# Kernel optimization log

Hardware: AMD Instinct MI355X
Metric: run time of the kernel (lower is better)

The kernel has to match this reference:

```python
import jax, jax.numpy as jnp
import numpy as np

N_NODES = 50000
N_EDGES = 800000
NUM_FEATURES = 256
HIDDEN = 128
NUM_CLASSES = 64


def gcn_conv(x, edge_index, W, b):
    """PyG-style GCNConv: out = D^-1/2 (A+I) D^-1/2 (x W) + b.

    edge_index[0] = source (j), edge_index[1] = target (i);
    messages flow source -> target and are summed at the target.
    """
    n = x.shape[0]
    loop = jnp.arange(n, dtype=edge_index.dtype)
    src = jnp.concatenate([edge_index[0], loop])  # [E+N]
    dst = jnp.concatenate([edge_index[1], loop])  # [E+N]

    h = x @ W  # [N, out_dim] — transform before propagate, as in PyG GCNConv

    deg = jax.ops.segment_sum(jnp.ones_like(dst, dtype=h.dtype), dst, num_segments=n)
    dinv = jnp.where(deg > 0, jax.lax.rsqrt(deg), 0.0)
    norm = dinv[src] * dinv[dst]  # [E+N]

    out = jax.ops.segment_sum(norm[:, None] * h[src], dst, num_segments=n)
    return out + b


def setup_inputs() -> dict:
    key = jax.random.key(0)
    k1, k2, k3, k4 = jax.random.split(key, 4)
    x = jax.random.normal(k1, (N_NODES, NUM_FEATURES), dtype=jnp.float32)
    edge_index = jax.random.randint(k2, (2, N_EDGES), 0, N_NODES, dtype=jnp.int64)
    # Glorot-style init for the two GCN layer weights, zero bias (PyG default)
    W1 = jax.random.normal(k3, (NUM_FEATURES, HIDDEN), dtype=jnp.float32) * (1.0 / np.sqrt(NUM_FEATURES))
    b1 = jnp.zeros((HIDDEN,), dtype=jnp.float32)
    W2 = jax.random.normal(k4, (HIDDEN, NUM_CLASSES), dtype=jnp.float32) * (1.0 / np.sqrt(HIDDEN))
    b2 = jnp.zeros((NUM_CLASSES,), dtype=jnp.float32)
    return {"x": x, "edge_index": edge_index, "W1": W1, "b1": b1, "W2": W2, "b2": b2}


def reference(x, edge_index, W1, b1, W2, b2):
    h = gcn_conv(x, edge_index, W1, b1)
    h = jax.nn.relu(h)
    # dropout(p=0.5, training=True): fixed key stands in for torch RNG
    keep = jax.random.bernoulli(jax.random.key(42), 0.5, h.shape)
    h = jnp.where(keep, h * 2.0, 0.0)
    out = gcn_conv(h, edge_index, W2, b2)
    return out
```

## Files before the change

### kernel.cpp

```cpp
#include <hip/hip_runtime.h>


typedef __attribute__((ext_vector_type(8))) short bf16x8;
typedef __attribute__((ext_vector_type(4))) float f32x4;
typedef __attribute__((ext_vector_type(8))) unsigned short us8;

__device__ __forceinline__ unsigned tf_rotl(unsigned x, int d) {
    return (x << d) | (x >> (32 - d));
}

__device__ __forceinline__ bool dropout_keep(unsigned flat_idx) {
    const unsigned K0 = 0u, K1 = 42u;
    const unsigned K2 = K0 ^ K1 ^ 0x1BD11BDAu;
    unsigned x0 = 0u, x1 = flat_idx;
    x0 += K0; x1 += K1;
#define TF_R(r) { x0 += x1; x1 = tf_rotl(x1, (r)); x1 ^= x0; }
    TF_R(13) TF_R(15) TF_R(26) TF_R(6)
    x0 += K1; x1 += K2 + 1u;
    TF_R(17) TF_R(29) TF_R(16) TF_R(24)
    x0 += K2; x1 += K0 + 2u;
    TF_R(13) TF_R(15) TF_R(26) TF_R(6)
    x0 += K0; x1 += K1 + 3u;
    TF_R(17) TF_R(29) TF_R(16) TF_R(24)
    x0 += K1; x1 += K2 + 4u;
    TF_R(13) TF_R(15) TF_R(26) TF_R(6)
    x0 += K2; x1 += K0 + 5u;
#undef TF_R
    return (((x0 ^ x1) >> 31) & 1u) == 0u;
}

__device__ __forceinline__ unsigned short bf16_rn(float x) {
    unsigned u = __float_as_uint(x);
    unsigned r = u + 0x7FFFu + ((u >> 16) & 1u);
    return (unsigned short)(r >> 16);
}
__device__ __forceinline__ void split_bf16(float x, unsigned short& h, unsigned short& l) {
    h = bf16_rn(x);
    float fh = __uint_as_float(((unsigned)h) << 16);
    l = bf16_rn(x - fh);
}
__device__ __forceinline__ void split4(float4 v, ushort4& h, ushort4& l) {
    unsigned short h0, h1, h2, h3, l0, l1, l2, l3;
    split_bf16(v.x, h0, l0); split_bf16(v.y, h1, l1);
    split_bf16(v.z, h2, l2); split_bf16(v.w, h3, l3);
    h = make_ushort4(h0, h1, h2, h3);
    l = make_ushort4(l0, l1, l2, l3);
}

__device__ __forceinline__ int ei_stride(const int* __restrict__ ei) {
    bool i64 = true;
#pragma unroll
    for (int k = 1; k <= 15; k += 2) i64 = i64 && (ei[k] == 0);
    return i64 ? 2 : 1;
}

__global__ void count_slot(const int* __restrict__ ei, unsigned* __restrict__ deg,
                           unsigned* __restrict__ aux, int E) {
    int e = blockIdx.x * blockDim.x + threadIdx.x;
    if (e >= E) return;
    size_t st = ei_stride(ei);
    aux[e] = atomicAdd(&deg[ei[((size_t)E + e) * st]], 1u);
}

__global__ __launch_bounds__(256)
void scan_phase1(const unsigned* __restrict__ deg, unsigned* __restrict__ blockSums,
                 float* __restrict__ dinv, int N) {
    const int i = blockIdx.x * 256 + threadIdx.x;
    const int lane = threadIdx.x & 63, wave = threadIdx.x >> 6;
    unsigned v = 0;
    if (i < N) {
        unsigned d = deg[i];
        v = (d + 7u) & ~7u;
        dinv[i] = rsqrtf((float)(d + 1u));
    }
    unsigned s = v;
#pragma unroll
    for (int o = 32; o > 0; o >>= 1) s += __shfl_down(s, o, 64);
    __shared__ unsigned ws[4];
    if (lane == 0) ws[wave] = s;
    __syncthreads();
    if (threadIdx.x == 0)
        blockSums[blockIdx.x] = ws[0] + ws[1] + ws[2] + ws[3];
}

__global__ __launch_bounds__(1024)
void scan_phase2(unsigned* __restrict__ blockSums, int nb) {
    __shared__ unsigned s[1024];
    const int t = threadIdx.x;
    unsigned v = (t < nb) ? blockSums[t] : 0u;
    s[t] = v;
    __syncthreads();
    for (int off = 1; off < 1024; off <<= 1) {
        unsigned u = (t >= off) ? s[t - off] : 0u;
        __syncthreads();
        s[t] += u;
        __syncthreads();
    }
    if (t < nb) blockSums[t] = s[t] - v;
}

__global__ __launch_bounds__(256)
void scan_phase3(const unsigned* __restrict__ deg, const unsigned* __restrict__ blockSums,
                 unsigned* __restrict__ rowptr, int* __restrict__ csr, int N) {
    const int i = blockIdx.x * 256 + threadIdx.x;
    const int t = threadIdx.x;
    unsigned d = 0, v = 0;
    if (i < N) {
        d = deg[i];
        v = (d + 7u) & ~7u;
    }
    __shared__ unsigned s[256];
    s[t] = v;
    __syncthreads();
    for (int off = 1; off < 256; off <<= 1) {
        unsigned u = (t >= off) ? s[t - off] : 0u;
        __syncthreads();
        s[t] += u;
        __syncthreads();
    }
    const unsigned incl = s[t];
    const unsigned off0 = blockSums[blockIdx.x];
    if (i < N) {
        const unsigned rp = off0 + incl - v;
        rowptr[i] = rp;
        if (i == N - 1) rowptr[N] = off0 + incl;
        for (unsigned u = d; u < v; ++u) csr[rp + u] = N;
    }
}

__global__ void place_edges(const int* __restrict__ ei, const unsigned* __restrict__ rowptr,
                            const unsigned* __restrict__ aux, int* __restrict__ csr, int E) {
    int e = blockIdx.x * blockDim.x + threadIdx.x;
    if (e >= E) return;
    size_t st = ei_stride(ei);
    int s = ei[(size_t)e * st];
    int d = ei[((size_t)E + e) * st];
    csr[rowptr[d] + aux[e]] = s;
}

__global__ void split_both(const float* __restrict__ W1, const float* __restrict__ W2,
                           unsigned short* __restrict__ wT1_hi, unsigned short* __restrict__ wT1_lo,
                           unsigned short* __restrict__ wT2_hi, unsigned short* __restrict__ wT2_lo) {
    int idx = blockIdx.x * blockDim.x + threadIdx.x;
    unsigned short h, l;
    if (idx < 256 * 128) {
        int k = idx / 128, n = idx % 128;
        split_bf16(W1[idx], h, l);
        wT1_hi[(size_t)n * 256 + k] = h;
        wT1_lo[(size_t)n * 256 + k] = l;
    } else if (idx < 256 * 128 + 128 * 64) {
        int j = idx - 256 * 128;
        int k = j / 64, n = j % 64;
        split_bf16(W2[j], h, l);
        wT2_hi[(size_t)n * 128 + k] = h;
        wT2_lo[(size_t)n * 128 + k] = l;
    }
}

template <int K_, int NOUT_, bool SPLITA>
__global__ __launch_bounds__(256)
void gemm_mfma(const void* __restrict__ Xv, const unsigned short* __restrict__ wT_hi,
               const unsigned short* __restrict__ wT_lo, const float* __restrict__ scale,
               unsigned short* __restrict__ Yb, int nrows) {
    constexpr int BM = 64, BK = 32, NKT = K_ / BK;
    constexpr int CT = NOUT_ / 64;
    constexpr int LDW = BK + 8;
    constexpr int WPT = NOUT_ / 32;

    __shared__ __attribute__((aligned(16))) unsigned short xs_hi[BM][LDW];
    __shared__ __attribute__((aligned(16))) unsigned short xs_lo[SPLITA ? BM : 1][SPLITA ? LDW : 1];
    __shared__ __attribute__((aligned(16))) unsigned short ws_hi[NOUT_][LDW];
    __shared__ __attribute__((aligned(16))) unsigned short ws_lo[NOUT_][LDW];

    const int t = threadIdx.x;
    const int wave = t >> 6, lane = t & 63;
    const int m16 = lane & 15, kg = lane >> 4;
    const int row0 = blockIdx.x * BM;
    const int n0 = wave * (16 * CT);

    if (blockIdx.x == 0 && t < NOUT_ / 8) {
        us8 z = (us8)0;
        *(us8*)&Yb[(size_t)nrows * NOUT_ + t * 8] = z;
    }

    const float* Xf = (const float*)Xv;
    const unsigned short* Xb = (const unsigned short*)Xv;

    f32x4 acc[4][CT];
#pragma unroll
    for (int r = 0; r < 4; ++r)
#pragma unroll
        for (int c = 0; c < CT; ++c) acc[r][c] = {0.f, 0.f, 0.f, 0.f};

    float4 xpre[2];
    us8 xpre_b;
    ushort4 wpre_h[WPT], wpre_l[WPT];

    if constexpr (SPLITA) {
#pragma unroll
        for (int i = 0; i < 2; ++i) {
            int idx = t + i * 256;
            int r = idx >> 3, c4 = idx & 7;
            int gr = row0 + r;
            xpre[i] = (gr < nrows) ? *(const float4*)&Xf[(size_t)gr * K_ + c4 * 4]
                                   : make_float4(0.f, 0.f, 0.f, 0.f);
        }
    } else {
        int r = t >> 2, c8 = t & 3;
        int gr = row0 + r;
        xpre_b = (gr < nrows) ? *(const us8*)&Xb[(size_t)gr * K_ + c8 * 8] : (us8)0;
    }
#pragma unroll
    for (int i = 0; i < WPT; ++i) {
        int idx = t + i * 256;
        int n = idx >> 3, c4 = idx & 7;
        wpre_h[i] = *(const ushort4*)&wT_hi[(size_t)n * K_ + c4 * 4];
        wpre_l[i] = *(const ushort4*)&wT_lo[(size_t)n * K_ + c4 * 4];
    }

    for (int kb = 0; kb < NKT; ++kb) {
        if constexpr (SPLITA) {
#pragma unroll
            for (int i = 0; i < 2; ++i) {
                int idx = t + i * 256;
                int r = idx >> 3, c4 = idx & 7;
                ushort4 h, l;
                split4(xpre[i], h, l);
                *(ushort4*)&xs_hi[r][c4 * 4] = h;
                *(ushort4*)&xs_lo[r][c4 * 4] = l;
            }
        } else {
            int r = t >> 2, c8 = t & 3;
            *(us8*)&xs_hi[r][c8 * 8] = xpre_b;
        }
#pragma unroll
        for (int i = 0; i < WPT; ++i) {
            int idx = t + i * 256;
            int n = idx >> 3, c4 = idx & 7;
            *(ushort4*)&ws_hi[n][c4 * 4] = wpre_h[i];
            *(ushort4*)&ws_lo[n][c4 * 4] = wpre_l[i];
        }
        __syncthreads();

        if (kb + 1 < NKT) {
            const int koff = (kb + 1) * BK;
            if constexpr (SPLITA) {
#pragma unroll
                for (int i = 0; i < 2; ++i) {
                    int idx = t + i * 256;
                    int r = idx >> 3, c4 = idx & 7;
                    int gr = row0 + r;
                    xpre[i] = (gr < nrows) ? *(const float4*)&Xf[(size_t)gr * K_ + koff + c4 * 4]
                                           : make_float4(0.f, 0.f, 0.f, 0.f);
                }
            } else {
                int r = t >> 2, c8 = t & 3;
                int gr = row0 + r;
                xpre_b = (gr < nrows) ? *(const us8*)&Xb[(size_t)gr * K_ + koff + c8 * 8] : (us8)0;
            }
#pragma unroll
            for (int i = 0; i < WPT; ++i) {
                int idx = t + i * 256;
                int n = idx >> 3, c4 = idx & 7;
                wpre_h[i] = *(const ushort4*)&wT_hi[(size_t)n * K_ + koff + c4 * 4];
                wpre_l[i] = *(const ushort4*)&wT_lo[(size_t)n * K_ + koff + c4 * 4];
            }
        }

        bf16x8 bh[CT], bl[CT];
#pragma unroll
        for (int c = 0; c < CT; ++c) {
            bh[c] = *(const bf16x8*)&ws_hi[n0 + c * 16 + m16][kg * 8];
            bl[c] = *(const bf16x8*)&ws_lo[n0 + c * 16 + m16][kg * 8];
        }
#pragma unroll
        for (int r = 0; r < 4; ++r) {
            bf16x8 ah = *(const bf16x8*)&xs_hi[r * 16 + m16][kg * 8];
            if constexpr (SPLITA) {
                bf16x8 al = *(const bf16x8*)&xs_lo[r * 16 + m16][kg * 8];
#pragma unroll
                for (int c = 0; c < CT; ++c) {
                    acc[r][c] = __builtin_amdgcn_mfma_f32_16x16x32_bf16(ah, bh[c], acc[r][c], 0, 0, 0);
                    acc[r][c] = __builtin_amdgcn_mfma_f32_16x16x32_bf16(ah, bl[c], acc[r][c], 0, 0, 0);
                    acc[r][c] = __builtin_amdgcn_mfma_f32_16x16x32_bf16(al, bh[c], acc[r][c], 0, 0, 0);
                }
            } else {
#pragma unroll
                for (int c = 0; c < CT; ++c) {
                    acc[r][c] = __builtin_amdgcn_mfma_f32_16x16x32_bf16(ah, bh[c], acc[r][c], 0, 0, 0);
                    acc[r][c] = __builtin_amdgcn_mfma_f32_16x16x32_bf16(ah, bl[c], acc[r][c], 0, 0, 0);
                }
            }
        }
        __syncthreads();
    }

#pragma unroll
    for (int r = 0; r < 4; ++r) {
#pragma unroll
        for (int j = 0; j < 4; ++j) {
            int gr = row0 + r * 16 + kg * 4 + j;
            if (gr < nrows) {
                float s = scale[gr];
#pragma unroll
                for (int c = 0; c < CT; ++c)
                    Yb[(size_t)gr * NOUT_ + n0 + c * 16 + m16] = bf16_rn(acc[r][c][j] * s);
            }
        }
    }
}

__global__ __launch_bounds__(256)
void gather_drop(const unsigned* __restrict__ hs , const int* __restrict__ csr,
                 const unsigned* __restrict__ rowptr, const float* __restrict__ dinv,
                 const float* __restrict__ bias, unsigned* __restrict__ outb ,
                 int N) {
    const int node = blockIdx.x * 4 + (threadIdx.x >> 6);
    if (node >= N) return;
    const int lane = threadIdx.x & 63;
    const unsigned beg = rowptr[node];
    const unsigned end = rowptr[node + 1];
    const float dn = dinv[node];

    unsigned v = hs[(size_t)node * 64 + lane];
    float ax = __uint_as_float(v << 16);
    float ay = __uint_as_float(v & 0xffff0000u);
    for (unsigned k = beg; k < end; k += 8) {
        int j[8];
#pragma unroll
        for (int u = 0; u < 8; ++u) j[u] = csr[k + u];
        unsigned w[8];
#pragma unroll
        for (int u = 0; u < 8; ++u) w[u] = hs[(size_t)j[u] * 64 + lane];
#pragma unroll
        for (int u = 0; u < 8; ++u) {
            ax += __uint_as_float(w[u] << 16);
            ay += __uint_as_float(w[u] & 0xffff0000u);
        }
    }
    const int f0 = 2 * lane;
    float o0 = fmaxf(dn * ax + bias[f0], 0.0f);
    float o1 = fmaxf(dn * ay + bias[f0 + 1], 0.0f);
    unsigned base = (unsigned)node * 128u + (unsigned)f0;
    o0 = dropout_keep(base) ? 2.0f * o0 : 0.0f;
    o1 = dropout_keep(base + 1u) ? 2.0f * o1 : 0.0f;
    outb[(size_t)node * 64 + lane] =
        (unsigned)bf16_rn(o0) | ((unsigned)bf16_rn(o1) << 16);
}

__global__ __launch_bounds__(256)
void gather_out(const unsigned short* __restrict__ hs , const int* __restrict__ csr,
                const unsigned* __restrict__ rowptr, const float* __restrict__ dinv,
                const float* __restrict__ bias, float* __restrict__ outp, int N) {
    const int node = blockIdx.x * 4 + (threadIdx.x >> 6);
    if (node >= N) return;
    const int lane = threadIdx.x & 63;
    const unsigned beg = rowptr[node];
    const unsigned end = rowptr[node + 1];
    const float dn = dinv[node];

    float acc = __uint_as_float(((unsigned)hs[(size_t)node * 64 + lane]) << 16);
    for (unsigned k = beg; k < end; k += 8) {
        int j[8];
#pragma unroll
        for (int u = 0; u < 8; ++u) j[u] = csr[k + u];
        unsigned short w[8];
#pragma unroll
        for (int u = 0; u < 8; ++u) w[u] = hs[(size_t)j[u] * 64 + lane];
#pragma unroll
        for (int u = 0; u < 8; ++u) acc += __uint_as_float(((unsigned)w[u]) << 16);
    }
    outp[(size_t)node * 64 + lane] = dn * acc + bias[lane];
}

extern "C" void kernel_launch(void* const* d_in, const int* in_sizes, int n_in,
                              void* d_out, int out_size, void* d_ws, size_t ws_size,
                              hipStream_t stream) {
    const float* x  = (const float*)d_in[0];
    const int*   ei = (const int*)d_in[1];
    const float* W1 = (const float*)d_in[2];
    const float* b1 = (const float*)d_in[3];
    const float* W2 = (const float*)d_in[4];
    const float* b2 = (const float*)d_in[5];
    float* out = (float*)d_out;

    const int Fdim = 256, Hdim = 128, Cdim = 64;
    const int N = in_sizes[0] / Fdim;
    const int E = in_sizes[1] / 2;
    const int CSR_CAP = E + 7 * N;
    const int NB = (N + 255) / 256;

    unsigned short* wT1_hi = (unsigned short*)d_ws;
    unsigned short* wT1_lo = wT1_hi + 256 * 128;
    unsigned short* wT2_hi = wT1_lo + 256 * 128;
    unsigned short* wT2_lo = wT2_hi + 128 * 64;
    unsigned short* buffA  = wT2_lo + 128 * 64;
    unsigned short* buffB  = buffA + (size_t)(N + 1) * Hdim;
    unsigned* deg    = (unsigned*)(buffB + (size_t)N * Hdim);
    float*    dinv   = (float*)(deg + N);
    unsigned* rowptr = (unsigned*)(dinv + N);
    unsigned* blockSums = rowptr + (N + 1);
    unsigned* aux    = blockSums + NB;
    int*      csr    = (int*)(aux + E);

    hipMemsetAsync(deg, 0, (size_t)N * sizeof(unsigned), stream);

    count_slot<<<(E + 255) / 256, 256, 0, stream>>>(ei, deg, aux, E);
    scan_phase1<<<NB, 256, 0, stream>>>(deg, blockSums, dinv, N);
    scan_phase2<<<1, 1024, 0, stream>>>(blockSums, NB);
    scan_phase3<<<NB, 256, 0, stream>>>(deg, blockSums, rowptr, csr, N);
    place_edges<<<(E + 255) / 256, 256, 0, stream>>>(ei, rowptr, aux, csr, E);

    split_both<<<(256 * 128 + 128 * 64 + 255) / 256, 256, 0, stream>>>(
        W1, W2, wT1_hi, wT1_lo, wT2_hi, wT2_lo);

    gemm_mfma<256, 128, true><<<(N + 63) / 64, 256, 0, stream>>>(x, wT1_hi, wT1_lo, dinv, buffA, N);
    gather_drop<<<(N + 3) / 4, 256, 0, stream>>>((const unsigned*)buffA, csr, rowptr, dinv, b1,
                                                 (unsigned*)buffB, N);

    gemm_mfma<128, 64, false><<<(N + 63) / 64, 256, 0, stream>>>(buffB, wT2_hi, wT2_lo, dinv, buffA, N);
    gather_out<<<(N + 3) / 4, 256, 0, stream>>>(buffA, csr, rowptr, dinv, b2, out, N);
}
```

Before: 246.8 us.

## Overlap GEMM1 with degree counting and store per-edge norm weights in CSR

The first GEMM no longer depends on dinv, so it is fused into one launch with the atomic degree-count blocks and can overlap with graph preprocessing. The per-edge weight dinv[s]*dinv[d] is precomputed into an int2 CSR entry, and the gathers apply it with FMAs; padding entries point at node 0 with weight 0 instead of a zero sentinel row. The weight split and the degree zeroing move into one prep kernel, and the scan is merged into two kernels, removing a memset and several launches. In exchange, CSR reads double in size in both gathers, and rounding changes because the scaling now happens after the bf16 store rather than before it.

```diff
diff --git a/kernel.cpp b/kernel.cpp
--- a/kernel.cpp
+++ b/kernel.cpp
@@ -54,114 +54,12 @@
     return i64 ? 2 : 1;
 }
 
-__global__ void count_slot(const int* __restrict__ ei, unsigned* __restrict__ deg,
-                           unsigned* __restrict__ aux, int E) {
-    int e = blockIdx.x * blockDim.x + threadIdx.x;
-    if (e >= E) return;
-    size_t st = ei_stride(ei);
-    aux[e] = atomicAdd(&deg[ei[((size_t)E + e) * st]], 1u);
-}
-
-__global__ __launch_bounds__(256)
-void scan_phase1(const unsigned* __restrict__ deg, unsigned* __restrict__ blockSums,
-                 float* __restrict__ dinv, int N) {
-    const int i = blockIdx.x * 256 + threadIdx.x;
-    const int lane = threadIdx.x & 63, wave = threadIdx.x >> 6;
-    unsigned v = 0;
-    if (i < N) {
-        unsigned d = deg[i];
-        v = (d + 7u) & ~7u;
-        dinv[i] = rsqrtf((float)(d + 1u));
-    }
-    unsigned s = v;
-#pragma unroll
-    for (int o = 32; o > 0; o >>= 1) s += __shfl_down(s, o, 64);
-    __shared__ unsigned ws[4];
-    if (lane == 0) ws[wave] = s;
-    __syncthreads();
-    if (threadIdx.x == 0)
-        blockSums[blockIdx.x] = ws[0] + ws[1] + ws[2] + ws[3];
-}
-
-__global__ __launch_bounds__(1024)
-void scan_phase2(unsigned* __restrict__ blockSums, int nb) {
-    __shared__ unsigned s[1024];
-    const int t = threadIdx.x;
-    unsigned v = (t < nb) ? blockSums[t] : 0u;
-    s[t] = v;
-    __syncthreads();
-    for (int off = 1; off < 1024; off <<= 1) {
-        unsigned u = (t >= off) ? s[t - off] : 0u;
-        __syncthreads();
-        s[t] += u;
-        __syncthreads();
-    }
-    if (t < nb) blockSums[t] = s[t] - v;
-}
-
-__global__ __launch_bounds__(256)
-void scan_phase3(const unsigned* __restrict__ deg, const unsigned* __restrict__ blockSums,
-                 unsigned* __restrict__ rowptr, int* __restrict__ csr, int N) {
-    const int i = blockIdx.x * 256 + threadIdx.x;
-    const int t = threadIdx.x;
-    unsigned d = 0, v = 0;
-    if (i < N) {
-        d = deg[i];
-        v = (d + 7u) & ~7u;
-    }
-    __shared__ unsigned s[256];
-    s[t] = v;
-    __syncthreads();
-    for (int off = 1; off < 256; off <<= 1) {
-        unsigned u = (t >= off) ? s[t - off] : 0u;
-        __syncthreads();
-        s[t] += u;
-        __syncthreads();
-    }
-    const unsigned incl = s[t];
-    const unsigned off0 = blockSums[blockIdx.x];
-    if (i < N) {
-        const unsigned rp = off0 + incl - v;
-        rowptr[i] = rp;
-        if (i == N - 1) rowptr[N] = off0 + incl;
-        for (unsigned u = d; u < v; ++u) csr[rp + u] = N;
-    }
-}
-
-__global__ void place_edges(const int* __restrict__ ei, const unsigned* __restrict__ rowptr,
-                            const unsigned* __restrict__ aux, int* __restrict__ csr, int E) {
-    int e = blockIdx.x * blockDim.x + threadIdx.x;
-    if (e >= E) return;
-    size_t st = ei_stride(ei);
-    int s = ei[(size_t)e * st];
-    int d = ei[((size_t)E + e) * st];
-    csr[rowptr[d] + aux[e]] = s;
-}
-
-__global__ void split_both(const float* __restrict__ W1, const float* __restrict__ W2,
-                           unsigned short* __restrict__ wT1_hi, unsigned short* __restrict__ wT1_lo,
-                           unsigned short* __restrict__ wT2_hi, unsigned short* __restrict__ wT2_lo) {
-    int idx = blockIdx.x * blockDim.x + threadIdx.x;
-    unsigned short h, l;
-    if (idx < 256 * 128) {
-        int k = idx / 128, n = idx % 128;
-        split_bf16(W1[idx], h, l);
-        wT1_hi[(size_t)n * 256 + k] = h;
-        wT1_lo[(size_t)n * 256 + k] = l;
-    } else if (idx < 256 * 128 + 128 * 64) {
-        int j = idx - 256 * 128;
-        int k = j / 64, n = j % 64;
-        split_bf16(W2[j], h, l);
-        wT2_hi[(size_t)n * 128 + k] = h;
-        wT2_lo[(size_t)n * 128 + k] = l;
-    }
-}
-
 template <int K_, int NOUT_, bool SPLITA>
-__global__ __launch_bounds__(256)
-void gemm_mfma(const void* __restrict__ Xv, const unsigned short* __restrict__ wT_hi,
-               const unsigned short* __restrict__ wT_lo, const float* __restrict__ scale,
-               unsigned short* __restrict__ Yb, int nrows) {
+__device__ __forceinline__ void gemm_core(const void* __restrict__ Xv,
+                                          const unsigned short* __restrict__ wT_hi,
+                                          const unsigned short* __restrict__ wT_lo,
+                                          unsigned short* __restrict__ Yb,
+                                          int nrows, int bid) {
     constexpr int BM = 64, BK = 32, NKT = K_ / BK;
     constexpr int CT = NOUT_ / 64;
     constexpr int LDW = BK + 8;
@@ -175,13 +73,8 @@
     const int t = threadIdx.x;
     const int wave = t >> 6, lane = t & 63;
     const int m16 = lane & 15, kg = lane >> 4;
-    const int row0 = blockIdx.x * BM;
+    const int row0 = bid * BM;
     const int n0 = wave * (16 * CT);
-
-    if (blockIdx.x == 0 && t < NOUT_ / 8) {
-        us8 z = (us8)0;
-        *(us8*)&Yb[(size_t)nrows * NOUT_ + t * 8] = z;
-    }
 
     const float* Xf = (const float*)Xv;
     const unsigned short* Xb = (const unsigned short*)Xv;
@@ -301,17 +194,138 @@
         for (int j = 0; j < 4; ++j) {
             int gr = row0 + r * 16 + kg * 4 + j;
             if (gr < nrows) {
-                float s = scale[gr];
 #pragma unroll
                 for (int c = 0; c < CT; ++c)
-                    Yb[(size_t)gr * NOUT_ + n0 + c * 16 + m16] = bf16_rn(acc[r][c][j] * s);
+                    Yb[(size_t)gr * NOUT_ + n0 + c * 16 + m16] = bf16_rn(acc[r][c][j]);
             }
         }
     }
 }
 
 __global__ __launch_bounds__(256)
-void gather_drop(const unsigned* __restrict__ hs , const int* __restrict__ csr,
+void prep(const float* __restrict__ W1, const float* __restrict__ W2,
+          unsigned short* __restrict__ wT1_hi, unsigned short* __restrict__ wT1_lo,
+          unsigned short* __restrict__ wT2_hi, unsigned short* __restrict__ wT2_lo,
+          unsigned* __restrict__ deg, int N) {
+    const int b = blockIdx.x, t = threadIdx.x;
+    if (b < 160) {
+        int idx = b * 256 + t;
+        unsigned short h, l;
+        if (idx < 256 * 128) {
+            int k = idx / 128, n = idx % 128;
+            split_bf16(W1[idx], h, l);
+            wT1_hi[(size_t)n * 256 + k] = h;
+            wT1_lo[(size_t)n * 256 + k] = l;
+        } else if (idx < 256 * 128 + 128 * 64) {
+            int j = idx - 256 * 128;
+            int k = j / 64, n = j % 64;
+            split_bf16(W2[j], h, l);
+            wT2_hi[(size_t)n * 128 + k] = h;
+            wT2_lo[(size_t)n * 128 + k] = l;
+        }
+    } else {
+        int i = (b - 160) * 256 + t;
+        if (i < N) deg[i] = 0;
+    }
+}
+
+__global__ __launch_bounds__(256)
+void mega1(const float* __restrict__ x, const unsigned short* __restrict__ wT1_hi,
+           const unsigned short* __restrict__ wT1_lo, unsigned short* __restrict__ buffA,
+           const int* __restrict__ ei, unsigned* __restrict__ deg,
+           unsigned* __restrict__ aux, int N, int E, int nGemm) {
+    if ((int)blockIdx.x < nGemm) {
+        gemm_core<256, 128, true>(x, wT1_hi, wT1_lo, buffA, N, blockIdx.x);
+        return;
+    }
+    int e = (blockIdx.x - nGemm) * 256 + threadIdx.x;
+    if (e >= E) return;
+    size_t st = ei_stride(ei);
+    aux[e] = atomicAdd(&deg[ei[((size_t)E + e) * st]], 1u);
+}
+
+__global__ __launch_bounds__(256)
+void scan_phase1(const unsigned* __restrict__ deg, unsigned* __restrict__ blockSums,
+                 float* __restrict__ dinv, int N) {
+    const int i = blockIdx.x * 256 + threadIdx.x;
+    const int lane = threadIdx.x & 63, wave = threadIdx.x >> 6;
+    unsigned v = 0;
+    if (i < N) {
+        unsigned d = deg[i];
+        v = (d + 7u) & ~7u;
+        dinv[i] = rsqrtf((float)(d + 1u));
+    }
+    unsigned s = v;
+#pragma unroll
+    for (int o = 32; o > 0; o >>= 1) s += __shfl_down(s, o, 64);
+    __shared__ unsigned ws[4];
+    if (lane == 0) ws[wave] = s;
+    __syncthreads();
+    if (threadIdx.x == 0)
+        blockSums[blockIdx.x] = ws[0] + ws[1] + ws[2] + ws[3];
+}
+
+__global__ __launch_bounds__(256)
+void scan_phase3b(const unsigned* __restrict__ deg, const unsigned* __restrict__ blockSums,
+                  unsigned* __restrict__ rowptr, int2* __restrict__ csr2, int N, int nb) {
+    __shared__ unsigned s[256];
+    const int t = threadIdx.x;
+
+    unsigned bsv = (t < nb) ? blockSums[t] : 0u;
+    s[t] = bsv;
+    __syncthreads();
+    for (int off = 1; off < 256; off <<= 1) {
+        unsigned u = (t >= off) ? s[t - off] : 0u;
+        __syncthreads();
+        s[t] += u;
+        __syncthreads();
+    }
+    const unsigned off0 = (blockIdx.x == 0) ? 0u : s[blockIdx.x - 1];
+    __syncthreads();
+
+    const int i = blockIdx.x * 256 + t;
+    unsigned d = 0, v = 0;
+    if (i < N) { d = deg[i]; v = (d + 7u) & ~7u; }
+    s[t] = v;
+    __syncthreads();
+    for (int off = 1; off < 256; off <<= 1) {
+        unsigned u = (t >= off) ? s[t - off] : 0u;
+        __syncthreads();
+        s[t] += u;
+        __syncthreads();
+    }
+    const unsigned incl = s[t];
+    if (i < N) {
+        const unsigned rp = off0 + incl - v;
+        rowptr[i] = rp;
+        if (i == N - 1) rowptr[N] = off0 + incl;
+        for (unsigned u = d; u < v; ++u) csr2[rp + u] = make_int2(0, 0);
+    }
+}
+
+__global__ void place_edges(const int* __restrict__ ei, const unsigned* __restrict__ rowptr,
+                            const unsigned* __restrict__ aux, const float* __restrict__ dinv,
+                            int2* __restrict__ csr2, int E) {
+    int e = blockIdx.x * blockDim.x + threadIdx.x;
+    if (e >= E) return;
+    size_t st = ei_stride(ei);
+    int s = ei[(size_t)e * st];
+    int d = ei[((size_t)E + e) * st];
+    int2 c;
+    c.x = s;
+    c.y = __float_as_int(dinv[s] * dinv[d]);
+    csr2[rowptr[d] + aux[e]] = c;
+}
+
+__global__ __launch_bounds__(256)
+void gemm2_kernel(const unsigned short* __restrict__ Xb, const unsigned short* __restrict__ wT_hi,
+                  const unsigned short* __restrict__ wT_lo, unsigned short* __restrict__ Yb,
+                  int nrows) {
+    gemm_core<128, 64, false>(Xb, wT_hi, wT_lo, Yb, nrows, blockIdx.x);
+}
+
+__global__ __launch_bounds__(256)
+void gather_drop(const unsigned* __restrict__ hs , const int2* __restrict__ csr2,
                  const unsigned* __restrict__ rowptr, const float* __restrict__ dinv,
                  const float* __restrict__ bias, unsigned* __restrict__ outb ,
                  int N) {
@@ -321,26 +335,28 @@
     const unsigned beg = rowptr[node];
     const unsigned end = rowptr[node + 1];
     const float dn = dinv[node];
+    const float dn2 = dn * dn;
 
     unsigned v = hs[(size_t)node * 64 + lane];
-    float ax = __uint_as_float(v << 16);
-    float ay = __uint_as_float(v & 0xffff0000u);
+    float ax = dn2 * __uint_as_float(v << 16);
+    float ay = dn2 * __uint_as_float(v & 0xffff0000u);
     for (unsigned k = beg; k < end; k += 8) {
-        int j[8];
-#pragma unroll
-        for (int u = 0; u < 8; ++u) j[u] = csr[k + u];
-        unsigned w[8];
-#pragma unroll
-        for (int u = 0; u < 8; ++u) w[u] = hs[(size_t)j[u] * 64 + lane];
+        int2 c[8];
+#pragma unroll
+        for (int u = 0; u < 8; ++u) c[u] = csr2[k + u];
+        unsigned w8[8];
+#pragma unroll
+        for (int u = 0; u < 8; ++u) w8[u] = hs[(size_t)c[u].x * 64 + lane];
 #pragma unroll
         for (int u = 0; u < 8; ++u) {
-            ax += __uint_as_float(w[u] << 16);
-            ay += __uint_as_float(w[u] & 0xffff0000u);
+            float w = __int_as_float(c[u].y);
+            ax = fmaf(w, __uint_as_float(w8[u] << 16), ax);
+            ay = fmaf(w, __uint_as_float(w8[u] & 0xffff0000u), ay);
         }
     }
     const int f0 = 2 * lane;
-    float o0 = fmaxf(dn * ax + bias[f0], 0.0f);
-    float o1 = fmaxf(dn * ay + bias[f0 + 1], 0.0f);
+    float o0 = fmaxf(ax + bias[f0], 0.0f);
+    float o1 = fmaxf(ay + bias[f0 + 1], 0.0f);
     unsigned base = (unsigned)node * 128u + (unsigned)f0;
     o0 = dropout_keep(base) ? 2.0f * o0 : 0.0f;
     o1 = dropout_keep(base + 1u) ? 2.0f * o1 : 0.0f;
@@ -349,7 +365,7 @@
 }
 
 __global__ __launch_bounds__(256)
-void gather_out(const unsigned short* __restrict__ hs , const int* __restrict__ csr,
+void gather_out(const unsigned short* __restrict__ hs , const int2* __restrict__ csr2,
                 const unsigned* __restrict__ rowptr, const float* __restrict__ dinv,
                 const float* __restrict__ bias, float* __restrict__ outp, int N) {
     const int node = blockIdx.x * 4 + (threadIdx.x >> 6);
@@ -359,18 +375,19 @@
     const unsigned end = rowptr[node + 1];
     const float dn = dinv[node];
 
-    float acc = __uint_as_float(((unsigned)hs[(size_t)node * 64 + lane]) << 16);
+    float acc = dn * dn * __uint_as_float(((unsigned)hs[(size_t)node * 64 + lane]) << 16);
     for (unsigned k = beg; k < end; k += 8) {
-        int j[8];
-#pragma unroll
-        for (int u = 0; u < 8; ++u) j[u] = csr[k + u];
-        unsigned short w[8];
-#pragma unroll
-        for (int u = 0; u < 8; ++u) w[u] = hs[(size_t)j[u] * 64 + lane];
-#pragma unroll
-        for (int u = 0; u < 8; ++u) acc += __uint_as_float(((unsigned)w[u]) << 16);
-    }
-    outp[(size_t)node * 64 + lane] = dn * acc + bias[lane];
+        int2 c[8];
+#pragma unroll
+        for (int u = 0; u < 8; ++u) c[u] = csr2[k + u];
+        unsigned short w8[8];
+#pragma unroll
+        for (int u = 0; u < 8; ++u) w8[u] = hs[(size_t)c[u].x * 64 + lane];
+#pragma unroll
+        for (int u = 0; u < 8; ++u)
+            acc = fmaf(__int_as_float(c[u].y), __uint_as_float(((unsigned)w8[u]) << 16), acc);
+    }
+    outp[(size_t)node * 64 + lane] = acc + bias[lane];
 }
 
 extern "C" void kernel_launch(void* const* d_in, const int* in_sizes, int n_in,
@@ -395,29 +412,26 @@
     unsigned short* wT2_hi = wT1_lo + 256 * 128;
     unsigned short* wT2_lo = wT2_hi + 128 * 64;
     unsigned short* buffA  = wT2_lo + 128 * 64;
-    unsigned short* buffB  = buffA + (size_t)(N + 1) * Hdim;
+    unsigned short* buffB  = buffA + (size_t)N * Hdim;
     unsigned* deg    = (unsigned*)(buffB + (size_t)N * Hdim);
     float*    dinv   = (float*)(deg + N);
     unsigned* rowptr = (unsigned*)(dinv + N);
     unsigned* blockSums = rowptr + (N + 1);
     unsigned* aux    = blockSums + NB;
-    int*      csr    = (int*)(aux + E);
-
-    hipMemsetAsync(deg, 0, (size_t)N * sizeof(unsigned), stream);
-
-    count_slot<<<(E + 255) / 256, 256, 0, stream>>>(ei, deg, aux, E);
+    uintptr_t csr_p  = ((uintptr_t)(aux + E) + 15) & ~(uintptr_t)15;
+    int2*     csr2   = (int2*)csr_p;
+
+    const int nGemm1 = (N + 63) / 64;
+    const int nCount = (E + 255) / 256;
+
+    prep<<<160 + (N + 255) / 256, 256, 0, stream>>>(W1, W2, wT1_hi, wT1_lo, wT2_hi, wT2_lo, deg, N);
+    mega1<<<nGemm1 + nCount, 256, 0, stream>>>(x, wT1_hi, wT1_lo, buffA, ei, deg, aux, N, E, nGemm1);
     scan_phase1<<<NB, 256, 0, stream>>>(deg, blockSums, dinv, N);
-    scan_phase2<<<1, 1024, 0, stream>>>(blockSums, NB);
-    scan_phase3<<<NB, 256, 0, stream>>>(deg, blockSums, rowptr, csr, N);
-    place_edges<<<(E + 255) / 256, 256, 0, stream>>>(ei, rowptr, aux, csr, E);
-
-    split_both<<<(256 * 128 + 128 * 64 + 255) / 256, 256, 0, stream>>>(
-        W1, W2, wT1_hi, wT1_lo, wT2_hi, wT2_lo);
-
-    gemm_mfma<256, 128, true><<<(N + 63) / 64, 256, 0, stream>>>(x, wT1_hi, wT1_lo, dinv, buffA, N);
-    gather_drop<<<(N + 3) / 4, 256, 0, stream>>>((const unsigned*)buffA, csr, rowptr, dinv, b1,
+    scan_phase3b<<<NB, 256, 0, stream>>>(deg, blockSums, rowptr, csr2, N, NB);
+    place_edges<<<nCount, 256, 0, stream>>>(ei, rowptr, aux, dinv, csr2, E);
+
+    gather_drop<<<(N + 3) / 4, 256, 0, stream>>>((const unsigned*)buffA, csr2, rowptr, dinv, b1,
                                                  (unsigned*)buffB, N);
-
-    gemm_mfma<128, 64, false><<<(N + 63) / 64, 256, 0, stream>>>(buffB, wT2_hi, wT2_lo, dinv, buffA, N);
-    gather_out<<<(N + 3) / 4, 256, 0, stream>>>(buffA, csr, rowptr, dinv, b2, out, N);
-}
+    gemm2_kernel<<<(N + 63) / 64, 256, 0, stream>>>(buffB, wT2_hi, wT2_lo, buffA, N);
+    gather_out<<<(N + 3) / 4, 256, 0, stream>>>(buffA, csr2, rowptr, dinv, b2, out, N);
+}
```

Result: no change. 247.4 us (+0.2%).
